# Kernel tuning notes

Hardware: AMD Instinct MI355X
Metric: run time of the kernel (lower is better)

The kernel has to match this reference:

```python
import jax, jax.numpy as jnp
import numpy as np

B, T, C, H = 16, 4096, 256, 256

def setup_inputs() -> dict:
    key = jax.random.key(0)
    kx, kwi, kbi, kwh, kbh = jax.random.split(key, 5)
    s = 1.0 / np.sqrt(C)
    return {
        "x": jax.random.normal(kx, (B, T, C), dtype=jnp.float32),
        "Wi": jax.random.uniform(kwi, (H, C), dtype=jnp.float32, minval=-s, maxval=s),
        "bi": jax.random.uniform(kbi, (H,), dtype=jnp.float32, minval=-s, maxval=s),
        "Wh": jax.random.uniform(kwh, (H, H), dtype=jnp.float32, minval=-s, maxval=s),
        "bh": jax.random.uniform(kbh, (H,), dtype=jnp.float32, minval=-s, maxval=s),
    }

def reference(x, Wi, bi, Wh, bh):
    # Faithful to the source: Cell computes tanh(i2h(x) + h2h(x)) -- both
    # linears applied to x_t, the hidden state is never consumed, so there
    # is no recurrence and all timesteps can be computed in one fused pass.
    # hidden_states: [B, T, H]
    hidden_states = jnp.tanh(
        jnp.einsum("btc,hc->bth", x, Wi) + bi
        + jnp.einsum("btc,hc->bth", x, Wh) + bh
    )
    h_last = hidden_states[:, -1, :]  # h after the loop
    return (hidden_states, h_last)
```

## Files before the change

kernel.cpp:

```cpp
#include <hip/hip_runtime.h>
#include <hip/hip_bf16.h>


using short8 = __attribute__((ext_vector_type(8))) short;
using f32x4  = __attribute__((ext_vector_type(4))) float;

constexpr int Bn = 16, Tn = 4096, Cn = 256, Hn = 256;
constexpr int Mn = Bn * Tn;
constexpr int BM = 128, BK = 64;

__device__ inline unsigned pack2_bf16(float a, float b) {
  unsigned ua = __float_as_uint(a);
  unsigned ub = __float_as_uint(b);
  ua += 0x7fffu + ((ua >> 16) & 1u);
  ub += 0x7fffu + ((ub >> 16) & 1u);
  return (ua >> 16) | (ub & 0xffff0000u);
}

__global__ __launch_bounds__(256) void prep_kernel(
    const float* __restrict__ Wi, const float* __restrict__ bi,
    const float* __restrict__ Wh, const float* __restrict__ bh,
    unsigned short* __restrict__ Wc, float* __restrict__ bc) {
  int idx = blockIdx.x * 256 + threadIdx.x;
  float w = Wi[idx] + Wh[idx];
  unsigned u = __float_as_uint(w);
  u += 0x7fffu + ((u >> 16) & 1u);
  Wc[idx] = (unsigned short)(u >> 16);
  if (blockIdx.x == 0) bc[threadIdx.x] = bi[threadIdx.x] + bh[threadIdx.x];
}

__global__ __launch_bounds__(256, 2) void gemm_tanh_kernel(
    const float* __restrict__ x, const unsigned short* __restrict__ Wc,
    const float* __restrict__ bc, float* __restrict__ out) {
  __shared__ __align__(16) unsigned short Asm[BM * BK];
  __shared__ __align__(16) unsigned short Bsm[256 * BK];

  const int tid  = threadIdx.x;
  const int lane = tid & 63;
  const int wave = tid >> 6;
  const int wm   = wave >> 1;
  const int wn   = wave & 1;
  const int rid  = lane & 15;
  const int kgrp = lane >> 4;
  const int mBase = blockIdx.x * BM;

  f32x4 acc[4][8];
#pragma unroll
  for (int i = 0; i < 4; i++)
#pragma unroll
    for (int j = 0; j < 8; j++) acc[i][j] = (f32x4)0.f;

  for (int k0 = 0; k0 < Cn; k0 += BK) {
#pragma unroll
    for (int i = 0; i < 4; i++) {
      int h = i * 256 + tid;
      int r = h >> 3;
      int c = h & 7;
      const float4* src =
          (const float4*)(x + (size_t)(mBase + r) * Cn + k0) + c * 2;
      float4 v0 = src[0];
      float4 v1 = src[1];
      uint4 p;
      p.x = pack2_bf16(v0.x, v0.y);
      p.y = pack2_bf16(v0.z, v0.w);
      p.z = pack2_bf16(v1.x, v1.y);
      p.w = pack2_bf16(v1.z, v1.w);
      int pc = c ^ (r & 7);
      *(uint4*)&Asm[(r << 6) + (pc << 3)] = p;
    }
#pragma unroll
    for (int i = 0; i < 8; i++) {
      int h = i * 256 + tid;
      int r = h >> 3;
      int c = h & 7;
      uint4 v = *(const uint4*)(Wc + r * Cn + k0 + c * 8);
      int pc = c ^ (r & 7);
      *(uint4*)&Bsm[(r << 6) + (pc << 3)] = v;
    }
    __syncthreads();

#pragma unroll
    for (int khalf = 0; khalf < 2; khalf++) {
      const int chunk = (khalf << 2) | kgrp;
      short8 af[4], bf[8];
#pragma unroll
      for (int im = 0; im < 4; im++) {
        int row = wm * 64 + im * 16 + rid;
        af[im] = *(const short8*)&Asm[(row << 6) + ((chunk ^ (rid & 7)) << 3)];
      }
#pragma unroll
      for (int in = 0; in < 8; in++) {
        int row = wn * 128 + in * 16 + rid;
        bf[in] = *(const short8*)&Bsm[(row << 6) + ((chunk ^ (rid & 7)) << 3)];
      }
#pragma unroll
      for (int im = 0; im < 4; im++)
#pragma unroll
        for (int in = 0; in < 8; in++)
          acc[im][in] = __builtin_amdgcn_mfma_f32_16x16x32_bf16(
              af[im], bf[in], acc[im][in], 0, 0, 0);
    }
    __syncthreads();
  }

#pragma unroll
  for (int in = 0; in < 8; in++) {
    int n = wn * 128 + in * 16 + rid;
    float bias = bc[n];
#pragma unroll
    for (int im = 0; im < 4; im++) {
      int mrow = mBase + wm * 64 + im * 16 + kgrp * 4;
#pragma unroll
      for (int r = 0; r < 4; r++) {
        int m = mrow + r;
        float v = acc[im][in][r] + bias;
        float t = 1.f - 2.f / (__expf(2.f * v) + 1.f);
        out[(size_t)m * Hn + n] = t;
        if ((m & (Tn - 1)) == (Tn - 1))
          out[(size_t)Mn * Hn + (size_t)(m >> 12) * Hn + n] = t;
      }
    }
  }
}

extern "C" void kernel_launch(void* const* d_in, const int* in_sizes, int n_in,
                              void* d_out, int out_size, void* d_ws,
                              size_t ws_size, hipStream_t stream) {
  (void)in_sizes; (void)n_in; (void)out_size; (void)ws_size;
  const float* x  = (const float*)d_in[0];
  const float* Wi = (const float*)d_in[1];
  const float* bi = (const float*)d_in[2];
  const float* Wh = (const float*)d_in[3];
  const float* bh = (const float*)d_in[4];
  float* out = (float*)d_out;

  unsigned short* Wc = (unsigned short*)d_ws;
  float* bc = (float*)((char*)d_ws + (size_t)Hn * Cn * sizeof(unsigned short));

  prep_kernel<<<(Hn * Cn) / 256, 256, 0, stream>>>(Wi, bi, Wh, bh, Wc, bc);
  gemm_tanh_kernel<<<Mn / BM, 256, 0, stream>>>(x, Wc, bc, out);
}
```

Baseline: 134.2 us.

## Fuse weight prep into GEMM and keep full-K weight tile in LDS

```diff
diff --git a/kernel.cpp b/kernel.cpp
--- a/kernel.cpp
+++ b/kernel.cpp
@@ -1,13 +1,11 @@
 #include <hip/hip_runtime.h>
-#include <hip/hip_bf16.h>
 
 
 using short8 = __attribute__((ext_vector_type(8))) short;
 using f32x4  = __attribute__((ext_vector_type(4))) float;
 
-constexpr int Bn = 16, Tn = 4096, Cn = 256, Hn = 256;
-constexpr int Mn = Bn * Tn;
-constexpr int BM = 128, BK = 64;
+constexpr int Tn = 4096, Cn = 256, Hn = 256;
+constexpr int Mn = 16 * Tn;
 
 __device__ inline unsigned pack2_bf16(float a, float b) {
   unsigned ua = __float_as_uint(a);
@@ -17,99 +15,91 @@
   return (ua >> 16) | (ub & 0xffff0000u);
 }
 
-__global__ __launch_bounds__(256) void prep_kernel(
-    const float* __restrict__ Wi, const float* __restrict__ bi,
-    const float* __restrict__ Wh, const float* __restrict__ bh,
-    unsigned short* __restrict__ Wc, float* __restrict__ bc) {
-  int idx = blockIdx.x * 256 + threadIdx.x;
-  float w = Wi[idx] + Wh[idx];
-  unsigned u = __float_as_uint(w);
-  u += 0x7fffu + ((u >> 16) & 1u);
-  Wc[idx] = (unsigned short)(u >> 16);
-  if (blockIdx.x == 0) bc[threadIdx.x] = bi[threadIdx.x] + bh[threadIdx.x];
-}
+union u4s8 { uint4 u; short8 s; };
 
-__global__ __launch_bounds__(256, 2) void gemm_tanh_kernel(
-    const float* __restrict__ x, const unsigned short* __restrict__ Wc,
-    const float* __restrict__ bc, float* __restrict__ out) {
-  __shared__ __align__(16) unsigned short Asm[BM * BK];
-  __shared__ __align__(16) unsigned short Bsm[256 * BK];
+__global__ __launch_bounds__(512, 4) void fused_gemm_tanh(
+    const float* __restrict__ x, const float* __restrict__ Wi,
+    const float* __restrict__ bi, const float* __restrict__ Wh,
+    const float* __restrict__ bh, float* __restrict__ out) {
+  __shared__ __align__(16) unsigned short Bsm[128 * 256];
 
-  const int tid  = threadIdx.x;
+  const int tid   = threadIdx.x;
+  const int mb    = blockIdx.x >> 1;
+  const int nb    = blockIdx.x & 1;
+  const int mBase = mb * 256;
+  const int nBase = nb * 128;
+
+#pragma unroll
+  for (int i = 0; i < 8; i++) {
+    int h = i * 512 + tid;
+    int r = h >> 5;
+    int c = h & 31;
+    const float4* wi4 = (const float4*)(Wi + (size_t)(nBase + r) * Cn + c * 8);
+    const float4* wh4 = (const float4*)(Wh + (size_t)(nBase + r) * Cn + c * 8);
+    float4 a0 = wi4[0], a1 = wi4[1];
+    float4 b0 = wh4[0], b1 = wh4[1];
+    uint4 p;
+    p.x = pack2_bf16(a0.x + b0.x, a0.y + b0.y);
+    p.y = pack2_bf16(a0.z + b0.z, a0.w + b0.w);
+    p.z = pack2_bf16(a1.x + b1.x, a1.y + b1.y);
+    p.w = pack2_bf16(a1.z + b1.z, a1.w + b1.w);
+    int pc = c ^ (r & 7);
+    *(uint4*)&Bsm[(r << 8) + (pc << 3)] = p;
+  }
+  __syncthreads();
+
+  const int wave = tid >> 6;
   const int lane = tid & 63;
-  const int wave = tid >> 6;
-  const int wm   = wave >> 1;
-  const int wn   = wave & 1;
   const int rid  = lane & 15;
   const int kgrp = lane >> 4;
-  const int mBase = blockIdx.x * BM;
+  const int rowBase = mBase + wave * 32;
 
-  f32x4 acc[4][8];
+  f32x4 acc[2][8];
 #pragma unroll
-  for (int i = 0; i < 4; i++)
+  for (int im = 0; im < 2; im++)
 #pragma unroll
-    for (int j = 0; j < 8; j++) acc[i][j] = (f32x4)0.f;
+    for (int in = 0; in < 8; in++) acc[im][in] = (f32x4)0.f;
 
-  for (int k0 = 0; k0 < Cn; k0 += BK) {
+  const float* a0p = x + (size_t)(rowBase + rid) * Cn + kgrp * 8;
+  const float* a1p = a0p + (size_t)16 * Cn;
+
+#pragma unroll 2
+  for (int kc = 0; kc < 8; kc++) {
+    short8 af[2];
+    {
+      const float4* p0 = (const float4*)(a0p + kc * 32);
+      const float4* p1 = (const float4*)(a1p + kc * 32);
+      float4 v0 = p0[0], v1 = p0[1];
+      float4 w0 = p1[0], w1 = p1[1];
+      u4s8 t0, t1;
+      t0.u.x = pack2_bf16(v0.x, v0.y); t0.u.y = pack2_bf16(v0.z, v0.w);
+      t0.u.z = pack2_bf16(v1.x, v1.y); t0.u.w = pack2_bf16(v1.z, v1.w);
+      t1.u.x = pack2_bf16(w0.x, w0.y); t1.u.y = pack2_bf16(w0.z, w0.w);
+      t1.u.z = pack2_bf16(w1.x, w1.y); t1.u.w = pack2_bf16(w1.z, w1.w);
+      af[0] = t0.s; af[1] = t1.s;
+    }
+    short8 bf[8];
+    const int cbase = (kc << 2) | kgrp;
 #pragma unroll
-    for (int i = 0; i < 4; i++) {
-      int h = i * 256 + tid;
-      int r = h >> 3;
-      int c = h & 7;
-      const float4* src =
-          (const float4*)(x + (size_t)(mBase + r) * Cn + k0) + c * 2;
-      float4 v0 = src[0];
-      float4 v1 = src[1];
-      uint4 p;
-      p.x = pack2_bf16(v0.x, v0.y);
-      p.y = pack2_bf16(v0.z, v0.w);
-      p.z = pack2_bf16(v1.x, v1.y);
-      p.w = pack2_bf16(v1.z, v1.w);
-      int pc = c ^ (r & 7);
-      *(uint4*)&Asm[(r << 6) + (pc << 3)] = p;
+    for (int in = 0; in < 8; in++) {
+      int ln = in * 16 + rid;
+      bf[in] = *(const short8*)&Bsm[(ln << 8) + ((cbase ^ (ln & 7)) << 3)];
     }
 #pragma unroll
-    for (int i = 0; i < 8; i++) {
-      int h = i * 256 + tid;
-      int r = h >> 3;
-      int c = h & 7;
-      uint4 v = *(const uint4*)(Wc + r * Cn + k0 + c * 8);
-      int pc = c ^ (r & 7);
-      *(uint4*)&Bsm[(r << 6) + (pc << 3)] = v;
-    }
-    __syncthreads();
-
+    for (int im = 0; im < 2; im++)
 #pragma unroll
-    for (int khalf = 0; khalf < 2; khalf++) {
-      const int chunk = (khalf << 2) | kgrp;
-      short8 af[4], bf[8];
-#pragma unroll
-      for (int im = 0; im < 4; im++) {
-        int row = wm * 64 + im * 16 + rid;
-        af[im] = *(const short8*)&Asm[(row << 6) + ((chunk ^ (rid & 7)) << 3)];
-      }
-#pragma unroll
-      for (int in = 0; in < 8; in++) {
-        int row = wn * 128 + in * 16 + rid;
-        bf[in] = *(const short8*)&Bsm[(row << 6) + ((chunk ^ (rid & 7)) << 3)];
-      }
-#pragma unroll
-      for (int im = 0; im < 4; im++)
-#pragma unroll
-        for (int in = 0; in < 8; in++)
-          acc[im][in] = __builtin_amdgcn_mfma_f32_16x16x32_bf16(
-              af[im], bf[in], acc[im][in], 0, 0, 0);
-    }
-    __syncthreads();
+      for (int in = 0; in < 8; in++)
+        acc[im][in] = __builtin_amdgcn_mfma_f32_16x16x32_bf16(
+            af[im], bf[in], acc[im][in], 0, 0, 0);
   }
 
 #pragma unroll
   for (int in = 0; in < 8; in++) {
-    int n = wn * 128 + in * 16 + rid;
-    float bias = bc[n];
+    int n = nBase + in * 16 + rid;
+    float bias = bi[n] + bh[n];
 #pragma unroll
-    for (int im = 0; im < 4; im++) {
-      int mrow = mBase + wm * 64 + im * 16 + kgrp * 4;
+    for (int im = 0; im < 2; im++) {
+      int mrow = rowBase + im * 16 + kgrp * 4;
 #pragma unroll
       for (int r = 0; r < 4; r++) {
         int m = mrow + r;
@@ -126,7 +116,7 @@
 extern "C" void kernel_launch(void* const* d_in, const int* in_sizes, int n_in,
                               void* d_out, int out_size, void* d_ws,
                               size_t ws_size, hipStream_t stream) {
-  (void)in_sizes; (void)n_in; (void)out_size; (void)ws_size;
+  (void)in_sizes; (void)n_in; (void)out_size; (void)d_ws; (void)ws_size;
   const float* x  = (const float*)d_in[0];
   const float* Wi = (const float*)d_in[1];
   const float* bi = (const float*)d_in[2];
@@ -134,9 +124,5 @@
   const float* bh = (const float*)d_in[4];
   float* out = (float*)d_out;
 
-  unsigned short* Wc = (unsigned short*)d_ws;
-  float* bc = (float*)((char*)d_ws + (size_t)Hn * Cn * sizeof(unsigned short));
-
-  prep_kernel<<<(Hn * Cn) / 256, 256, 0, stream>>>(Wi, bi, Wh, bh, Wc, bc);
-  gemm_tanh_kernel<<<Mn / BM, 256, 0, stream>>>(x, Wc, bc, out);
+  fused_gemm_tanh<<<512, 512, 0, stream>>>(x, Wi, bi, Wh, bh, out);
 }
```

Result: slower. 142.9 us (+6.5%).
